# Optimization experiments

Measured on AMD Instinct MI355X. Metric: run time of the kernel, lower is better.

## Reference

```python
import jax, jax.numpy as jnp
import numpy as np

EPS = 1e-5
NUM_GROUPS = 32


def setup_inputs() -> dict:
    key = jax.random.key(0)
    B, C, H, W = 16, 512, 32, 32
    ks = jax.random.split(key, 5)
    s = 1.0 / np.sqrt(C)  # keep attention logits well-scaled
    return {
        "x": jax.random.normal(ks[0], (B, C, H, W), jnp.float32),
        "gamma": jnp.ones((C,), jnp.float32),
        "beta": jnp.zeros((C,), jnp.float32),
        "wq": jax.random.normal(ks[1], (C, C), jnp.float32) * s,
        "bq": jnp.zeros((C,), jnp.float32),
        "wk": jax.random.normal(ks[2], (C, C), jnp.float32) * s,
        "bk": jnp.zeros((C,), jnp.float32),
        "wv": jax.random.normal(ks[3], (C, C), jnp.float32) * s,
        "bv": jnp.zeros((C,), jnp.float32),
        "wp": jax.random.normal(ks[4], (C, C), jnp.float32) * s,
        "bp": jnp.zeros((C,), jnp.float32),
    }


def _group_norm(x, gamma, beta):
    B, C, H, W = x.shape
    g = NUM_GROUPS
    xg = x.reshape(B, g, C // g, H * W)
    mu = jnp.mean(xg, axis=(2, 3), keepdims=True)
    var = jnp.mean(jnp.square(xg - mu), axis=(2, 3), keepdims=True)
    h = (xg - mu) * jax.lax.rsqrt(var + EPS)
    h = h.reshape(B, C, H, W)
    return h * gamma[None, :, None, None] + beta[None, :, None, None]


def reference(x, gamma, beta, wq, bq, wk, bk, wv, bv, wp, bp):
    B, C, H, W = x.shape
    N = H * W
    h = _group_norm(x, gamma, beta).reshape(B, C, N)  # [B,C,N]
    # 1x1 convs == per-pixel matmuls over channels
    q = jnp.einsum('oc,bcn->bon', wq, h) + bq[None, :, None]
    k = jnp.einsum('oc,bcn->bon', wk, h) + bk[None, :, None]
    v = jnp.einsum('oc,bcn->bon', wv, h) + bv[None, :, None]
    scale = int(C) ** (-0.5)
    logits = jnp.einsum('bcn,bcm->bnm', q, k) * scale  # [B,N,N]
    attn = jax.nn.softmax(logits, axis=-1)
    o = jnp.einsum('bnm,bcm->bcn', attn, v)  # [B,C,N]
    out = jnp.einsum('oc,bcn->bon', wp, o) + bp[None, :, None]
    return x + out.reshape(B, C, H, W)
```

## Files before the change

kernel.cpp:

```cpp
#include <hip/hip_runtime.h>
#include <hip/hip_bf16.h>

typedef __attribute__((ext_vector_type(8))) short bf16x8;
typedef __attribute__((ext_vector_type(4))) float f32x4;
typedef __attribute__((ext_vector_type(8))) unsigned short u16x8;
typedef __attribute__((ext_vector_type(4))) unsigned short u16x4;

static __device__ __forceinline__ unsigned short f2bf(float f) {
  __hip_bfloat16 h = __float2bfloat16(f);
  union { __hip_bfloat16 h; unsigned short u; } cv; cv.h = h; return cv.u;
}
static __device__ __forceinline__ float bf2f(unsigned short u) {
  union { unsigned int u; float f; } cv; cv.u = ((unsigned int)u) << 16; return cv.f;
}

static __device__ __forceinline__ void gload16(const unsigned short* g, unsigned short* l) {
  __builtin_amdgcn_global_load_lds((const __attribute__((address_space(1))) void*)g,
                                   (__attribute__((address_space(3))) void*)l, 16, 0, 0);
}

#define BK 32

__global__ __launch_bounds__(256, 4) void gemm_bt(
    const unsigned short* __restrict__ A, const unsigned short* __restrict__ Bm,
    long sA, long sB, int lda, int ldb, int K,
    const float* __restrict__ bias, int bias_mode, float post_scale,
    unsigned short* __restrict__ D, long sD, int ldd)
{
  __shared__ unsigned short lA[2][128 * BK];
  __shared__ unsigned short lB[2][128 * BK];
  const int gx = gridDim.x, gy = gridDim.y;
  const int nwg = gx * gy * gridDim.z;
  int orig = blockIdx.x + gx * (blockIdx.y + gy * blockIdx.z);
  int id = (orig & 7) * (nwg >> 3) + (orig >> 3);
  const int bxi = id % gx;
  int rem = id / gx;
  const int byi = rem % gy;
  const int bz = rem / gy;

  const int tid = threadIdx.x, lane = tid & 63, wid = tid >> 6;
  const int l15 = lane & 15, lhi = lane >> 4;
  const int wr = wid >> 1, wc = wid & 1;
  const long bm = (long)byi * 128, bn = (long)bxi * 128;
  const unsigned short* Ab = A + (size_t)bz * sA + (size_t)bm * lda;
  const unsigned short* Bb = Bm + (size_t)bz * sB + (size_t)bn * ldb;
  const int NT = K >> 5;

  f32x4 acc[4][4];
  #pragma unroll
  for (int i = 0; i < 4; ++i)
    #pragma unroll
    for (int j = 0; j < 4; ++j) acc[i][j] = (f32x4){0.f, 0.f, 0.f, 0.f};

  auto stage = [&](int buf, int k0) {
    #pragma unroll
    for (int j = 0; j < 2; ++j) {
      int bi = j * 256 + tid;
      int row = bi >> 2, sl = bi & 3;
      int kb = sl ^ ((row >> 1) & 3);
      gload16(Ab + (size_t)row * lda + k0 + kb * 8, &lA[buf][(j * 256 + wid * 64) * 8]);
    }
    #pragma unroll
    for (int j = 0; j < 2; ++j) {
      int bi = j * 256 + tid;
      int row = bi >> 2, sl = bi & 3;
      int kb = sl ^ ((row >> 1) & 3);
      gload16(Bb + (size_t)row * ldb + k0 + kb * 8, &lB[buf][(j * 256 + wid * 64) * 8]);
    }
  };

  stage(0, 0);
  __syncthreads();
  int buf = 0;
  for (int t = 0; t < NT; ++t) {
    if (t + 1 < NT) stage(buf ^ 1, (t + 1) * BK);
    bf16x8 af[4], bfr[4];
    #pragma unroll
    for (int mi = 0; mi < 4; ++mi) {
      int row = wr * 64 + mi * 16 + l15;
      int sl = lhi ^ ((row >> 1) & 3);
      af[mi] = *(const bf16x8*)&lA[buf][row * BK + sl * 8];
    }
    #pragma unroll
    for (int ni = 0; ni < 4; ++ni) {
      int row = wc * 64 + ni * 16 + l15;
      int sl = lhi ^ ((row >> 1) & 3);
      bfr[ni] = *(const bf16x8*)&lB[buf][row * BK + sl * 8];
    }
    #pragma unroll
    for (int mi = 0; mi < 4; ++mi)
      #pragma unroll
      for (int ni = 0; ni < 4; ++ni)
        acc[mi][ni] = __builtin_amdgcn_mfma_f32_16x16x32_bf16(af[mi], bfr[ni], acc[mi][ni], 0, 0, 0);
    __syncthreads();
    buf ^= 1;
  }

  #pragma unroll
  for (int mi = 0; mi < 4; ++mi) {
    #pragma unroll
    for (int ni = 0; ni < 4; ++ni) {
      #pragma unroll
      for (int r = 0; r < 4; ++r) {
        long row = bm + wr * 64 + mi * 16 + lhi * 4 + r;
        long col = bn + wc * 64 + ni * 16 + l15;
        float v = acc[mi][ni][r];
        if (bias_mode == 1) v += bias[row];
        else if (bias_mode == 2) v += bias[col];
        v *= post_scale;
        D[(size_t)bz * sD + (size_t)row * ldd + col] = f2bf(v);
      }
    }
  }
}

__global__ __launch_bounds__(256) void groupnorm_to_ht(
    const float* __restrict__ x, const float* __restrict__ gamma,
    const float* __restrict__ beta, unsigned short* __restrict__ ht)
{
  const int b = blockIdx.x >> 5;
  const int g = blockIdx.x & 31;
  const int tid = threadIdx.x, lane = tid & 63, wid = tid >> 6;
  const float4* xg4 = (const float4*)(x + ((size_t)b * 512 + g * 16) * 1024);
  float4 v[16];
  float s = 0.f, ss = 0.f;
  #pragma unroll
  for (int j = 0; j < 16; ++j) {
    v[j] = xg4[j * 256 + tid];
    s += v[j].x + v[j].y + v[j].z + v[j].w;
    ss += v[j].x * v[j].x + v[j].y * v[j].y + v[j].z * v[j].z + v[j].w * v[j].w;
  }
  #pragma unroll
  for (int o = 32; o; o >>= 1) { s += __shfl_xor(s, o); ss += __shfl_xor(ss, o); }
  __shared__ float red[8];
  if (lane == 0) { red[wid] = s; red[4 + wid] = ss; }
  __syncthreads();
  s = red[0] + red[1] + red[2] + red[3];
  ss = red[4] + red[5] + red[6] + red[7];
  const float mu = s * (1.f / 16384.f);
  const float var = ss * (1.f / 16384.f) - mu * mu;
  const float rsig = rsqrtf(var + 1e-5f);
  __shared__ unsigned short tile[16][1024];
  #pragma unroll
  for (int j = 0; j < 16; ++j) {
    int e = (j * 256 + tid) * 4;
    int ci = e >> 10, n = e & 1023;
    float ga = gamma[g * 16 + ci] * rsig, be = beta[g * 16 + ci];
    u16x4 o = { f2bf((v[j].x - mu) * ga + be), f2bf((v[j].y - mu) * ga + be),
                f2bf((v[j].z - mu) * ga + be), f2bf((v[j].w - mu) * ga + be) };
    *(u16x4*)&tile[ci][n] = o;
  }
  __syncthreads();
  unsigned short* hb = ht + (size_t)b * 1024 * 512 + g * 16;
  for (int rep = 0; rep < 4; ++rep) {
    int n = rep * 256 + tid;
    u16x8 lo, hi;
    #pragma unroll
    for (int ci = 0; ci < 8; ++ci) lo[ci] = tile[ci][n];
    #pragma unroll
    for (int ci = 0; ci < 8; ++ci) hi[ci] = tile[8 + ci][n];
    *(u16x8*)&hb[(size_t)n * 512] = lo;
    *(u16x8*)&hb[(size_t)n * 512 + 8] = hi;
  }
}

__global__ __launch_bounds__(256) void softmax_rows(unsigned short* __restrict__ attn)
{
  int row = blockIdx.x * 4 + (threadIdx.x >> 6);
  int lane = threadIdx.x & 63;
  unsigned short* p = attn + (size_t)row * 1024;
  u16x8 c0 = *(const u16x8*)&p[lane * 8];
  u16x8 c1 = *(const u16x8*)&p[512 + lane * 8];
  float f[16];
  #pragma unroll
  for (int j = 0; j < 8; ++j) { f[j] = bf2f(c0[j]); f[8 + j] = bf2f(c1[j]); }
  float m = f[0];
  #pragma unroll
  for (int j = 1; j < 16; ++j) m = fmaxf(m, f[j]);
  #pragma unroll
  for (int o = 32; o; o >>= 1) m = fmaxf(m, __shfl_xor(m, o));
  float sum = 0.f;
  #pragma unroll
  for (int j = 0; j < 16; ++j) { f[j] = __expf(f[j] - m); sum += f[j]; }
  #pragma unroll
  for (int o = 32; o; o >>= 1) sum += __shfl_xor(sum, o);
  float inv = 1.0f / sum;
  #pragma unroll
  for (int j = 0; j < 8; ++j) { c0[j] = f2bf(f[j] * inv); c1[j] = f2bf(f[8 + j] * inv); }
  *(u16x8*)&p[lane * 8] = c0;
  *(u16x8*)&p[512 + lane * 8] = c1;
}

__global__ __launch_bounds__(256) void residual_add(
    const float* __restrict__ x, const unsigned short* __restrict__ po,
    float* __restrict__ out)
{
  int t = blockIdx.x * 256 + threadIdx.x;
  int idx = t * 8;
  int b = idx >> 19, c = (idx >> 10) & 511, n = idx & 1023;
  u16x8 g = *(const u16x8*)&po[(size_t)c * 16384 + b * 1024 + n];
  float4 x0 = *(const float4*)&x[idx];
  float4 x1 = *(const float4*)&x[idx + 4];
  float4 o0 = { x0.x + bf2f(g[0]), x0.y + bf2f(g[1]), x0.z + bf2f(g[2]), x0.w + bf2f(g[3]) };
  float4 o1 = { x1.x + bf2f(g[4]), x1.y + bf2f(g[5]), x1.z + bf2f(g[6]), x1.w + bf2f(g[7]) };
  *(float4*)&out[idx] = o0;
  *(float4*)&out[idx + 4] = o1;
}

__global__ __launch_bounds__(256) void convert_weights(
    const float* __restrict__ wq, const float* __restrict__ wk,
    const float* __restrict__ wv, const float* __restrict__ wp,
    const float* __restrict__ bq, const float* __restrict__ bk,
    unsigned short* __restrict__ out, float* __restrict__ bqk)
{
  if (blockIdx.x == 1024) {
    int i = threadIdx.x * 4;
    if (i < 512) *(float4*)&bqk[i] = *(const float4*)&bq[i];
    else         *(float4*)&bqk[i] = *(const float4*)&bk[i - 512];
    return;
  }
  int t = blockIdx.x * 256 + threadIdx.x;
  int m = t >> 16;
  int off = (t & 65535) * 4;
  const float* src = m == 0 ? wq : m == 1 ? wk : m == 2 ? wv : wp;
  float4 v = *(const float4*)&src[off];
  u16x4 o = { f2bf(v.x), f2bf(v.y), f2bf(v.z), f2bf(v.w) };
  *(u16x4*)&out[(size_t)m * 262144 + off] = o;
}

extern "C" void kernel_launch(void* const* d_in, const int* in_sizes, int n_in,
                              void* d_out, int out_size, void* d_ws, size_t ws_size,
                              hipStream_t stream)
{
  const float* x     = (const float*)d_in[0];
  const float* gamma = (const float*)d_in[1];
  const float* beta  = (const float*)d_in[2];
  const float* wq    = (const float*)d_in[3];
  const float* bq    = (const float*)d_in[4];
  const float* wk    = (const float*)d_in[5];
  const float* bk    = (const float*)d_in[6];
  const float* wv    = (const float*)d_in[7];
  const float* bv    = (const float*)d_in[8];
  const float* wp    = (const float*)d_in[9];
  const float* bp    = (const float*)d_in[10];

  unsigned short* ws   = (unsigned short*)d_ws;
  unsigned short* w_bf = ws;
  unsigned short* ht   = w_bf + 1048576;
  unsigned short* qk   = ht + 8388608;
  unsigned short* vv2  = qk + 16777216;
  unsigned short* attn = vv2 + 8388608;
  unsigned short* ot   = attn + 16777216;
  float*          bqk  = (float*)(ot + 8388608);
  unsigned short* po   = attn;

  const float scale = 0.044194173824159216f;

  convert_weights<<<dim3(1025), dim3(256), 0, stream>>>(wq, wk, wv, wp, bq, bk, w_bf, bqk);
  groupnorm_to_ht<<<dim3(512), dim3(256), 0, stream>>>(x, gamma, beta, ht);

  gemm_bt<<<dim3(8, 128, 1), dim3(256), 0, stream>>>(
      ht, w_bf, 0L, 0L, 512, 512, 512,
      bqk, 2, 1.0f, qk, 0L, 1024);
  gemm_bt<<<dim3(128, 4, 1), dim3(256), 0, stream>>>(
      w_bf + 2 * 262144, ht, 0L, 0L, 512, 512, 512,
      bv, 1, 1.0f, vv2, 0L, 16384);
  gemm_bt<<<dim3(8, 8, 16), dim3(256), 0, stream>>>(
      qk, qk + 512, 1048576L, 1048576L, 1024, 1024, 512,
      (const float*)nullptr, 0, scale, attn, 1048576L, 1024);
  softmax_rows<<<dim3(4096), dim3(256), 0, stream>>>(attn);
  gemm_bt<<<dim3(4, 8, 16), dim3(256), 0, stream>>>(
      attn, vv2, 1048576L, 1024L, 1024, 16384, 1024,
      (const float*)nullptr, 0, 1.0f, ot, 524288L, 512);
  gemm_bt<<<dim3(128, 4, 1), dim3(256), 0, stream>>>(
      w_bf + 3 * 262144, ot, 0L, 0L, 512, 512, 512,
      bp, 1, 1.0f, po, 0L, 16384);
  residual_add<<<dim3(4096), dim3(256), 0, stream>>>(x, po, (float*)d_out);
}
```

Baseline: 185.7 us.

## Use single-buffered BK=64 K-tiles in GEMM instead of double-buffered BK=32

```diff
diff --git a/kernel.cpp b/kernel.cpp
--- a/kernel.cpp
+++ b/kernel.cpp
@@ -19,7 +19,7 @@
                                    (__attribute__((address_space(3))) void*)l, 16, 0, 0);
 }
 
-#define BK 32
+#define BK 64
 
 __global__ __launch_bounds__(256, 4) void gemm_bt(
     const unsigned short* __restrict__ A, const unsigned short* __restrict__ Bm,
@@ -27,8 +27,8 @@
     const float* __restrict__ bias, int bias_mode, float post_scale,
     unsigned short* __restrict__ D, long sD, int ldd)
 {
-  __shared__ unsigned short lA[2][128 * BK];
-  __shared__ unsigned short lB[2][128 * BK];
+  __shared__ unsigned short lA[128 * BK];
+  __shared__ unsigned short lB[128 * BK];
   const int gx = gridDim.x, gy = gridDim.y;
   const int nwg = gx * gy * gridDim.z;
   int orig = blockIdx.x + gx * (blockIdx.y + gy * blockIdx.z);
@@ -44,7 +44,7 @@
   const long bm = (long)byi * 128, bn = (long)bxi * 128;
   const unsigned short* Ab = A + (size_t)bz * sA + (size_t)bm * lda;
   const unsigned short* Bb = Bm + (size_t)bz * sB + (size_t)bn * ldb;
-  const int NT = K >> 5;
+  const int NT = K >> 6;
 
   f32x4 acc[4][4];
   #pragma unroll
@@ -52,48 +52,48 @@
     #pragma unroll
     for (int j = 0; j < 4; ++j) acc[i][j] = (f32x4){0.f, 0.f, 0.f, 0.f};
 
-  auto stage = [&](int buf, int k0) {
-    #pragma unroll
-    for (int j = 0; j < 2; ++j) {
+  auto stage = [&](int k0) {
+    #pragma unroll
+    for (int j = 0; j < 4; ++j) {
       int bi = j * 256 + tid;
-      int row = bi >> 2, sl = bi & 3;
-      int kb = sl ^ ((row >> 1) & 3);
-      gload16(Ab + (size_t)row * lda + k0 + kb * 8, &lA[buf][(j * 256 + wid * 64) * 8]);
-    }
-    #pragma unroll
-    for (int j = 0; j < 2; ++j) {
+      int row = bi >> 3, sl = bi & 7;
+      int kb = sl ^ (row & 7);
+      gload16(Ab + (size_t)row * lda + k0 + kb * 8, &lA[(j * 256 + wid * 64) * 8]);
+    }
+    #pragma unroll
+    for (int j = 0; j < 4; ++j) {
       int bi = j * 256 + tid;
-      int row = bi >> 2, sl = bi & 3;
-      int kb = sl ^ ((row >> 1) & 3);
-      gload16(Bb + (size_t)row * ldb + k0 + kb * 8, &lB[buf][(j * 256 + wid * 64) * 8]);
+      int row = bi >> 3, sl = bi & 7;
+      int kb = sl ^ (row & 7);
+      gload16(Bb + (size_t)row * ldb + k0 + kb * 8, &lB[(j * 256 + wid * 64) * 8]);
     }
   };
 
-  stage(0, 0);
-  __syncthreads();
-  int buf = 0;
   for (int t = 0; t < NT; ++t) {
-    if (t + 1 < NT) stage(buf ^ 1, (t + 1) * BK);
-    bf16x8 af[4], bfr[4];
-    #pragma unroll
-    for (int mi = 0; mi < 4; ++mi) {
-      int row = wr * 64 + mi * 16 + l15;
-      int sl = lhi ^ ((row >> 1) & 3);
-      af[mi] = *(const bf16x8*)&lA[buf][row * BK + sl * 8];
-    }
-    #pragma unroll
-    for (int ni = 0; ni < 4; ++ni) {
-      int row = wc * 64 + ni * 16 + l15;
-      int sl = lhi ^ ((row >> 1) & 3);
-      bfr[ni] = *(const bf16x8*)&lB[buf][row * BK + sl * 8];
-    }
-    #pragma unroll
-    for (int mi = 0; mi < 4; ++mi)
-      #pragma unroll
-      for (int ni = 0; ni < 4; ++ni)
-        acc[mi][ni] = __builtin_amdgcn_mfma_f32_16x16x32_bf16(af[mi], bfr[ni], acc[mi][ni], 0, 0, 0);
+    stage(t * BK);
     __syncthreads();
-    buf ^= 1;
+    #pragma unroll
+    for (int s = 0; s < 2; ++s) {
+      bf16x8 af[4], bfr[4];
+      #pragma unroll
+      for (int mi = 0; mi < 4; ++mi) {
+        int row = wr * 64 + mi * 16 + l15;
+        int sl = (s * 4 + lhi) ^ (row & 7);
+        af[mi] = *(const bf16x8*)&lA[row * BK + sl * 8];
+      }
+      #pragma unroll
+      for (int ni = 0; ni < 4; ++ni) {
+        int row = wc * 64 + ni * 16 + l15;
+        int sl = (s * 4 + lhi) ^ (row & 7);
+        bfr[ni] = *(const bf16x8*)&lB[row * BK + sl * 8];
+      }
+      #pragma unroll
+      for (int mi = 0; mi < 4; ++mi)
+        #pragma unroll
+        for (int ni = 0; ni < 4; ++ni)
+          acc[mi][ni] = __builtin_amdgcn_mfma_f32_16x16x32_bf16(af[mi], bfr[ni], acc[mi][ni], 0, 0, 0);
+    }
+    __syncthreads();
   }
 
   #pragma unroll
```

After: 172.8 us. 6.9% less time.
